# Kernel optimization log

Hardware: AMD Instinct MI355X
Metric: run time of the kernel (lower is better)

## Reference

```python
import jax, jax.numpy as jnp
import numpy as np

G, N, E = 4, 50000, 800000
F_IN, HID, OUT = 64, 128, 64


def setup_inputs() -> dict:
    key = jax.random.key(0)
    ks = jax.random.split(key, 4)
    x = jax.random.normal(ks[0], (G, N, F_IN), dtype=jnp.float32)
    edge_index = jax.random.randint(ks[1], (G, 2, E), 0, N)
    W1 = jax.random.normal(ks[2], (G, F_IN, HID), dtype=jnp.float32) / np.sqrt(F_IN).astype(np.float32)
    b1 = jnp.zeros((G, HID), dtype=jnp.float32)
    W2 = jax.random.normal(ks[3], (G, HID, OUT), dtype=jnp.float32) / np.sqrt(HID).astype(np.float32)
    b2 = jnp.zeros((G, OUT), dtype=jnp.float32)
    return {"x": x, "edge_index": edge_index, "W1": W1, "b1": b1, "W2": W2, "b2": b2}


def gcn_conv(x, src, dst, W, b):
    # PyG GCNConv: add self loops, symmetric norm D^-1/2 (A+I) D^-1/2, then XW + b
    n = x.shape[0]
    loop = jnp.arange(n)
    s = jnp.concatenate([src, loop])  # [E+N]
    d = jnp.concatenate([dst, loop])
    deg = jax.ops.segment_sum(jnp.ones_like(s, dtype=x.dtype), d, num_segments=n)
    dinv = jax.lax.rsqrt(deg)  # deg >= 1 because of self loops
    norm = dinv[s] * dinv[d]  # [E+N]
    h = x @ W  # [N, F_out]
    msg = h[s] * norm[:, None]  # edge-wise gather (memory-bound)
    out = jax.ops.segment_sum(msg, d, num_segments=n)  # scatter-add
    return out + b


def reference(x, edge_index, W1, b1, W2, b2):
    def per_graph(xg, eg, w1, b1g, w2, b2g):
        src, dst = eg[0], eg[1]
        h = jax.nn.elu(gcn_conv(xg, src, dst, w1, b1g))
        h = jax.nn.elu(gcn_conv(h, src, dst, w2, b2g))
        return h  # [N, OUT]

    out = jax.vmap(per_graph)(x, edge_index, W1, b1, W2, b2)  # [G, N, OUT]
    return out.reshape(G * N, OUT)  # torch.cat over graphs along dim 0
```

## Files before the change

### kernel.cpp

```cpp
#include <hip/hip_runtime.h>
#include <cstdint>

constexpr int G = 4, N = 50000, E = 800000;
constexpr int FIN = 64, HID = 128, FOUT = 64;
constexpr int NB = (N + 1023) / 1024;

constexpr int PB = 64;
constexpr int CP = E / PB;
constexpr int NBK = (N + 255) / 256;

typedef unsigned short ushort;
typedef _Float16 f16;

__device__ __forceinline__ ushort f2h(float f) {
  f16 h = (f16)f;
  return __builtin_bit_cast(ushort, h);
}
__device__ __forceinline__ float h2f(ushort u) {
  f16 h = __builtin_bit_cast(f16, u);
  return (float)h;
}

__device__ __forceinline__ void xcd_map(int b, int& g, int& chunk) {
  int xcd = b & 7;
  int sub = b >> 3;
  g = xcd >> 1;
  chunk = (xcd & 1) * 6250 + sub;
}

__global__ void k_x2h(const float4* __restrict__ X, const float* __restrict__ dinv,
                      ushort4* __restrict__ Xh, int n4) {
  int i = blockIdx.x * blockDim.x + threadIdx.x;
  if (i >= n4) return;
  float sc = dinv[i >> 4];
  float4 v = X[i];
  ushort4 o = {f2h(sc * v.x), f2h(sc * v.y), f2h(sc * v.z), f2h(sc * v.w)};
  Xh[i] = o;
}


__global__ __launch_bounds__(256) void k_phist(const int* __restrict__ ei,
                                               int* __restrict__ PH) {
  __shared__ int h[NBK];
  int pb = blockIdx.x, g = blockIdx.y;
  for (int i = threadIdx.x; i < NBK; i += 256) h[i] = 0;
  __syncthreads();
  const int4* dst4 = (const int4*)(ei + (size_t)g * 2 * E + E + (size_t)pb * CP);
  for (int i = threadIdx.x; i < CP / 4; i += 256) {
    int4 d = dst4[i];
    atomicAdd(&h[d.x >> 8], 1);
    atomicAdd(&h[d.y >> 8], 1);
    atomicAdd(&h[d.z >> 8], 1);
    atomicAdd(&h[d.w >> 8], 1);
  }
  __syncthreads();
  for (int i = threadIdx.x; i < NBK; i += 256)
    PH[((size_t)g * NBK + i) * PB + pb] = h[i];
}

__global__ void k_pscan(const int* __restrict__ PH, int* __restrict__ POFF,
                        int* __restrict__ BB) {
  int g = blockIdx.x, k = threadIdx.x;
  int tot = 0;
  if (k < NBK) {
#pragma unroll 8
    for (int pb = 0; pb < PB; ++pb) tot += PH[((size_t)g * NBK + k) * PB + pb];
  }
  __shared__ int sm[256];
  sm[k] = tot;
  __syncthreads();
  for (int off = 1; off < 256; off <<= 1) {
    int v = (k >= off) ? sm[k - off] : 0;
    __syncthreads();
    sm[k] += v;
    __syncthreads();
  }
  int excl = sm[k] - tot;
  if (k < NBK) {
    BB[g * (NBK + 1) + k] = excl;
    if (k == NBK - 1) BB[g * (NBK + 1) + NBK] = excl + tot;
    int run = excl;
#pragma unroll 8
    for (int pb = 0; pb < PB; ++pb) {
      POFF[((size_t)g * NBK + k) * PB + pb] = run;
      run += PH[((size_t)g * NBK + k) * PB + pb];
    }
  }
}

__global__ __launch_bounds__(256) void k_part(const int* __restrict__ ei,
                                              const int* __restrict__ POFF,
                                              unsigned* __restrict__ pairs) {
  __shared__ int off[NBK];
  __shared__ int rk[NBK];
  int pb = blockIdx.x, g = blockIdx.y;
  for (int i = threadIdx.x; i < NBK; i += 256) {
    off[i] = POFF[((size_t)g * NBK + i) * PB + pb];
    rk[i] = 0;
  }
  __syncthreads();
  const int* base = ei + (size_t)g * 2 * E + (size_t)pb * CP;
  const int4* s4 = (const int4*)base;
  const int4* d4 = (const int4*)(base + E);
  unsigned* pg = pairs + (size_t)g * E;
  for (int i = threadIdx.x; i < CP / 4; i += 256) {
    int4 s = s4[i], d = d4[i];
    int sv[4] = {s.x, s.y, s.z, s.w};
    int dv[4] = {d.x, d.y, d.z, d.w};
#pragma unroll
    for (int k = 0; k < 4; ++k) {
      int b = dv[k] >> 8;
      int r = atomicAdd(&rk[b], 1);
      pg[off[b] + r] = (unsigned)sv[k] | ((unsigned)(dv[k] & 255) << 16);
    }
  }
}

__global__ __launch_bounds__(256) void k_bcnt(const unsigned* __restrict__ pairs,
                                              const int* __restrict__ BB,
                                              int* __restrict__ cnt) {
  __shared__ int h[256];
  int k = blockIdx.x, g = blockIdx.y;
  h[threadIdx.x] = 0;
  __syncthreads();
  int lo = BB[g * (NBK + 1) + k], hi = BB[g * (NBK + 1) + k + 1];
  const unsigned* pg = pairs + (size_t)g * E;
  for (int i = lo + (int)threadIdx.x; i < hi; i += 256)
    atomicAdd(&h[(pg[i] >> 16) & 255], 1);
  __syncthreads();
  int n0 = k << 8;
  int nn = min(256, N - n0);
  if ((int)threadIdx.x < nn) cnt[g * N + n0 + threadIdx.x] = h[threadIdx.x];
}

__global__ __launch_bounds__(256) void k_place(const unsigned* __restrict__ pairs,
                                               const int* __restrict__ BB,
                                               const int* __restrict__ rowptr,
                                               int* __restrict__ col) {
  __shared__ int rp[256];
  __shared__ int rk[256];
  int k = blockIdx.x, g = blockIdx.y;
  int n0 = k << 8;
  int nn = min(256, N - n0);
  if ((int)threadIdx.x < nn) rp[threadIdx.x] = rowptr[g * (N + 1) + n0 + threadIdx.x];
  rk[threadIdx.x] = 0;
  __syncthreads();
  int lo = BB[g * (NBK + 1) + k], hi = BB[g * (NBK + 1) + k + 1];
  const unsigned* pg = pairs + (size_t)g * E;
  int* cg = col + (size_t)g * E;
  for (int i = lo + (int)threadIdx.x; i < hi; i += 256) {
    unsigned p = pg[i];
    int dl = (p >> 16) & 255;
    int r = atomicAdd(&rk[dl], 1);
    cg[rp[dl] + r] = (int)(p & 0xffffu);
  }
}

__global__ void k_scan_partial(const int* __restrict__ cnt, int* __restrict__ part) {
  int g = blockIdx.y, b = blockIdx.x, tid = threadIdx.x;
  int base = b * 1024 + tid * 4;
  int s = 0;
#pragma unroll
  for (int k = 0; k < 4; ++k) {
    int i = base + k;
    if (i < N) s += cnt[g * N + i];
  }
  __shared__ int sm[256];
  sm[tid] = s;
  __syncthreads();
  for (int off = 128; off > 0; off >>= 1) {
    if (tid < off) sm[tid] += sm[tid + off];
    __syncthreads();
  }
  if (tid == 0) part[g * NB + b] = sm[0];
}

__global__ void k_scan_mid(int* __restrict__ part, int* __restrict__ rowptr) {
  int g = blockIdx.x;
  if (threadIdx.x != 0) return;
  int run = 0;
  for (int b = 0; b < NB; ++b) {
    int t = part[g * NB + b];
    part[g * NB + b] = run;
    run += t;
  }
  rowptr[g * (N + 1) + N] = run;
}

__global__ void k_scan_final(const int* __restrict__ cnt, const int* __restrict__ part,
                             int* __restrict__ rowptr, float* __restrict__ dinv) {
  int g = blockIdx.y, b = blockIdx.x, tid = threadIdx.x;
  int base = b * 1024 + tid * 4;
  int c[4];
  int s = 0;
#pragma unroll
  for (int k = 0; k < 4; ++k) {
    int i = base + k;
    c[k] = (i < N) ? cnt[g * N + i] : 0;
    s += c[k];
  }
  __shared__ int sm[256];
  sm[tid] = s;
  __syncthreads();
  for (int off = 1; off < 256; off <<= 1) {
    int v = (tid >= off) ? sm[tid - off] : 0;
    __syncthreads();
    sm[tid] += v;
    __syncthreads();
  }
  int excl = sm[tid] - s + part[g * NB + b];
#pragma unroll
  for (int k = 0; k < 4; ++k) {
    int i = base + k;
    if (i < N) {
      rowptr[g * (N + 1) + i] = excl;
      dinv[g * N + i] = rsqrtf((float)(c[k] + 1));
    }
    excl += c[k];
  }
}

__global__ __launch_bounds__(256) void k_mlp(const float* __restrict__ X,
                                             const float* __restrict__ W1,
                                             const float* __restrict__ b1,
                                             const float* __restrict__ W2,
                                             const float* __restrict__ dinv,
                                             ushort* __restrict__ H2s) {
  constexpr int K = FIN;
  constexpr int PK = K + 1;
  __shared__ float lds[4 * 32 * 65];
  float* xs = lds;
  int g = blockIdx.y;
  int R0 = blockIdx.x * 64;
  for (int idx = threadIdx.x; idx < 64 * K; idx += 256) {
    int r = idx / K, k = idx - r * K;
    int row = R0 + r;
    xs[r * PK + k] = (row < N) ? X[((size_t)g * N + row) * K + k] : 0.f;
  }
  __syncthreads();
  int wv = threadIdx.x >> 6;
  int lane = threadIdx.x & 63;
  int c0 = __builtin_amdgcn_readfirstlane(wv * 32);
  const float* W1g = W1 + (size_t)g * K * HID;
  const float* xrow = &xs[lane * PK];
  float acc[32];
#pragma unroll
  for (int c = 0; c < 32; ++c) acc[c] = 0.f;
#pragma unroll 4
  for (int k = 0; k < K; ++k) {
    float xv = xrow[k];
#pragma unroll
    for (int c = 0; c < 32; ++c)
      acc[c] = fmaf(xv, W1g[(size_t)k * HID + c0 + c], acc[c]);
  }
#pragma unroll
  for (int c = 0; c < 32; ++c) {
    float v = acc[c] + b1[g * HID + c0 + c];
    acc[c] = v > 0.f ? v : expm1f(v);
  }
  const float* W2g = W2 + (size_t)g * HID * FOUT;
  int rrow = threadIdx.x >> 2;
  int jg = threadIdx.x & 3;
  for (int h = 0; h < 2; ++h) {
    float ph[32];
#pragma unroll
    for (int j = 0; j < 32; ++j) ph[j] = 0.f;
    for (int c = 0; c < 32; ++c) {
      const float* wr = &W2g[(size_t)(c0 + c) * FOUT + h * 32];
      float av = acc[c];
#pragma unroll
      for (int j = 0; j < 32; ++j) ph[j] = fmaf(av, wr[j], ph[j]);
    }
    __syncthreads();
#pragma unroll
    for (int j = 0; j < 32; ++j) lds[wv * 2080 + j * 65 + lane] = ph[j];
    __syncthreads();
    if (R0 + rrow < N) {
      float dd = dinv[g * N + R0 + rrow];
      ushort4 oa, ob;
      {
        int j = jg * 8;
        float s0 = lds[j * 65 + rrow] + lds[2080 + j * 65 + rrow] +
                   lds[4160 + j * 65 + rrow] + lds[6240 + j * 65 + rrow];
        float s1 = lds[(j + 1) * 65 + rrow] + lds[2080 + (j + 1) * 65 + rrow] +
                   lds[4160 + (j + 1) * 65 + rrow] + lds[6240 + (j + 1) * 65 + rrow];
        float s2 = lds[(j + 2) * 65 + rrow] + lds[2080 + (j + 2) * 65 + rrow] +
                   lds[4160 + (j + 2) * 65 + rrow] + lds[6240 + (j + 2) * 65 + rrow];
        float s3 = lds[(j + 3) * 65 + rrow] + lds[2080 + (j + 3) * 65 + rrow] +
                   lds[4160 + (j + 3) * 65 + rrow] + lds[6240 + (j + 3) * 65 + rrow];
        oa = {f2h(s0 * dd), f2h(s1 * dd), f2h(s2 * dd), f2h(s3 * dd)};
        float s4 = lds[(j + 4) * 65 + rrow] + lds[2080 + (j + 4) * 65 + rrow] +
                   lds[4160 + (j + 4) * 65 + rrow] + lds[6240 + (j + 4) * 65 + rrow];
        float s5 = lds[(j + 5) * 65 + rrow] + lds[2080 + (j + 5) * 65 + rrow] +
                   lds[4160 + (j + 5) * 65 + rrow] + lds[6240 + (j + 5) * 65 + rrow];
        float s6 = lds[(j + 6) * 65 + rrow] + lds[2080 + (j + 6) * 65 + rrow] +
                   lds[4160 + (j + 6) * 65 + rrow] + lds[6240 + (j + 6) * 65 + rrow];
        float s7 = lds[(j + 7) * 65 + rrow] + lds[2080 + (j + 7) * 65 + rrow] +
                   lds[4160 + (j + 7) * 65 + rrow] + lds[6240 + (j + 7) * 65 + rrow];
        ob = {f2h(s4 * dd), f2h(s5 * dd), f2h(s6 * dd), f2h(s7 * dd)};
      }
      ushort* dst = H2s + ((size_t)g * N + R0 + rrow) * FOUT + h * 32 + jg * 8;
      *(ushort4*)dst = oa;
      *(ushort4*)(dst + 4) = ob;
    }
  }
}

__device__ __forceinline__ float agg_row(const ushort* __restrict__ hb,
                                         const int* __restrict__ cl, int rs, int re,
                                         int lane, float acc) {
  int j = rs;
  for (; j + 16 <= re; j += 16) {
    int s[16];
#pragma unroll
    for (int k = 0; k < 16; ++k) s[k] = cl[j + k];
    float v[16];
#pragma unroll
    for (int k = 0; k < 16; ++k) v[k] = h2f(hb[(size_t)s[k] * 64 + lane]);
#pragma unroll
    for (int k = 0; k < 16; ++k) acc += v[k];
  }
  for (; j + 8 <= re; j += 8) {
    int s[8];
#pragma unroll
    for (int k = 0; k < 8; ++k) s[k] = cl[j + k];
    float v[8];
#pragma unroll
    for (int k = 0; k < 8; ++k) v[k] = h2f(hb[(size_t)s[k] * 64 + lane]);
#pragma unroll
    for (int k = 0; k < 8; ++k) acc += v[k];
  }
  for (; j < re; ++j) acc += h2f(hb[(size_t)cl[j] * 64 + lane]);
  return acc;
}

template <int F>
__global__ __launch_bounds__(256) void k_agg_in(const ushort* __restrict__ Xh,
                                                const int* __restrict__ rowptr,
                                                const int* __restrict__ col,
                                                const float* __restrict__ dinv,
                                                float* __restrict__ Z) {
  int g, chunk;
  xcd_map(blockIdx.x, g, chunk);
  int d = __builtin_amdgcn_readfirstlane(chunk * 4 + (threadIdx.x >> 6));
  int lane = threadIdx.x & 63;
  const ushort* hb = Xh + (size_t)g * N * F;
  const int* cl = col + (size_t)g * E;
  int rs = rowptr[g * (N + 1) + d];
  int re = rowptr[g * (N + 1) + d + 1];
  float acc = h2f(hb[(size_t)d * F + lane]);
  acc = agg_row(hb, cl, rs, re, lane, acc);
  Z[((size_t)g * N + d) * F + lane] = dinv[g * N + d] * acc;
}

template <int F>
__global__ __launch_bounds__(256) void k_agg_out(const ushort* __restrict__ Hsrc,
                                                 const int* __restrict__ rowptr,
                                                 const int* __restrict__ col,
                                                 const float* __restrict__ dinv,
                                                 const float* __restrict__ bias,
                                                 float* __restrict__ out) {
  int g, chunk;
  xcd_map(blockIdx.x, g, chunk);
  int d = __builtin_amdgcn_readfirstlane(chunk * 4 + (threadIdx.x >> 6));
  int lane = threadIdx.x & 63;
  const ushort* hb = Hsrc + (size_t)g * N * F;
  const int* cl = col + (size_t)g * E;
  int rs = rowptr[g * (N + 1) + d];
  int re = rowptr[g * (N + 1) + d + 1];
  float acc = h2f(hb[(size_t)d * F + lane]);
  acc = agg_row(hb, cl, rs, re, lane, acc);
  float p = acc * dinv[g * N + d] + bias[g * F + lane];
  p = p > 0.f ? p : expm1f(p);
  out[((size_t)g * N + d) * F + lane] = p;
}

extern "C" void kernel_launch(void* const* d_in, const int* in_sizes, int n_in,
                              void* d_out, int out_size, void* d_ws, size_t ws_size,
                              hipStream_t stream) {
  const float* x = (const float*)d_in[0];
  const int* ei = (const int*)d_in[1];
  const float* W1 = (const float*)d_in[2];
  const float* b1 = (const float*)d_in[3];
  const float* W2 = (const float*)d_in[4];
  const float* b2 = (const float*)d_in[5];
  float* out = (float*)d_out;

  char* p = (char*)d_ws;
  auto alloc = [&](size_t bytes) {
    char* r = p;
    p += (bytes + 255) & ~(size_t)255;
    return r;
  };
  int* cnt = (int*)alloc(sizeof(int) * G * N);
  int* rowptr = (int*)alloc(sizeof(int) * G * (N + 1));
  int* part = (int*)alloc(sizeof(int) * G * NB);
  float* dinv = (float*)alloc(sizeof(float) * G * N);
  int* col = (int*)alloc(sizeof(int) * (size_t)G * E);
  float* z = (float*)alloc(sizeof(float) * (size_t)G * N * FIN);
  char* scratch = (char*)alloc((size_t)103 << 20);
  ushort* h2s = (ushort*)z;
  unsigned* pairs = (unsigned*)scratch;
  int* PH = (int*)(scratch + ((size_t)13 << 20));
  int* POFF = (int*)(scratch + ((size_t)14 << 20));
  int* BB = (int*)(scratch + ((size_t)15 << 20));
  ushort* xh = (ushort*)(scratch + ((size_t)32 << 20));

  k_phist<<<dim3(PB, G), 256, 0, stream>>>(ei, PH);
  k_pscan<<<G, 256, 0, stream>>>(PH, POFF, BB);
  k_part<<<dim3(PB, G), 256, 0, stream>>>(ei, POFF, pairs);
  k_bcnt<<<dim3(NBK, G), 256, 0, stream>>>(pairs, BB, cnt);
  dim3 sg(NB, G);
  k_scan_partial<<<sg, 256, 0, stream>>>(cnt, part);
  k_scan_mid<<<G, 64, 0, stream>>>(part, rowptr);
  k_scan_final<<<sg, 256, 0, stream>>>(cnt, part, rowptr, dinv);
  k_place<<<dim3(NBK, G), 256, 0, stream>>>(pairs, BB, rowptr, col);

  k_x2h<<<(G * N * FIN / 4 + 255) / 256, 256, 0, stream>>>(
      (const float4*)x, dinv, (ushort4*)xh, G * N * FIN / 4);

  k_agg_in<FIN><<<(G * N) / 4, 256, 0, stream>>>(xh, rowptr, col, dinv, z);

  dim3 gg((N + 63) / 64, G);
  k_mlp<<<gg, 256, 0, stream>>>(z, W1, b1, W2, dinv, h2s);

  k_agg_out<FOUT><<<(G * N) / 4, 256, 0, stream>>>(h2s, rowptr, col, dinv, b2, out);
}
```

Measured before the change: 483.5 us.

## Stage layer-1 activations in LDS as fp16 and split second GEMM by output columns

In the fused MLP kernel, each wave used to compute a partial product over its 32 hidden channels for all 64 outputs, then reduce the four partials through a large fp32 LDS buffer in two passes. Now each wave writes its ELU-activated hidden values to LDS as packed fp16. Each wave then computes 16 output columns over the full hidden dimension, which removes the cross-wave reduction, one barrier pair and most of the LDS footprint. Launch bounds now ask for 8 blocks per CU to raise occupancy. The hidden activations pass through fp16 before the second matmul, which adds a small precision loss.

```diff
diff --git a/kernel.cpp b/kernel.cpp
--- a/kernel.cpp
+++ b/kernel.cpp
@@ -220,29 +220,29 @@
   }
 }
 
-__global__ __launch_bounds__(256) void k_mlp(const float* __restrict__ X,
-                                             const float* __restrict__ W1,
-                                             const float* __restrict__ b1,
-                                             const float* __restrict__ W2,
-                                             const float* __restrict__ dinv,
-                                             ushort* __restrict__ H2s) {
+__global__ __launch_bounds__(256, 8) void k_mlp(const float* __restrict__ X,
+                                                const float* __restrict__ W1,
+                                                const float* __restrict__ b1,
+                                                const float* __restrict__ W2,
+                                                const float* __restrict__ dinv,
+                                                ushort* __restrict__ H2s) {
   constexpr int K = FIN;
   constexpr int PK = K + 1;
-  __shared__ float lds[4 * 32 * 65];
-  float* xs = lds;
+  __shared__ float lds[64 * PK];
+  ushort* h1s = (ushort*)lds;
   int g = blockIdx.y;
   int R0 = blockIdx.x * 64;
   for (int idx = threadIdx.x; idx < 64 * K; idx += 256) {
-    int r = idx / K, k = idx - r * K;
+    int r = idx >> 6, k = idx & 63;
     int row = R0 + r;
-    xs[r * PK + k] = (row < N) ? X[((size_t)g * N + row) * K + k] : 0.f;
+    lds[r * PK + k] = (row < N) ? X[((size_t)g * N + row) * K + k] : 0.f;
   }
   __syncthreads();
   int wv = threadIdx.x >> 6;
   int lane = threadIdx.x & 63;
   int c0 = __builtin_amdgcn_readfirstlane(wv * 32);
   const float* W1g = W1 + (size_t)g * K * HID;
-  const float* xrow = &xs[lane * PK];
+  const float* xrow = &lds[lane * PK];
   float acc[32];
 #pragma unroll
   for (int c = 0; c < 32; ++c) acc[c] = 0.f;
@@ -258,51 +258,39 @@
     float v = acc[c] + b1[g * HID + c0 + c];
     acc[c] = v > 0.f ? v : expm1f(v);
   }
-  const float* W2g = W2 + (size_t)g * HID * FOUT;
-  int rrow = threadIdx.x >> 2;
-  int jg = threadIdx.x & 3;
-  for (int h = 0; h < 2; ++h) {
-    float ph[32];
-#pragma unroll
-    for (int j = 0; j < 32; ++j) ph[j] = 0.f;
-    for (int c = 0; c < 32; ++c) {
-      const float* wr = &W2g[(size_t)(c0 + c) * FOUT + h * 32];
-      float av = acc[c];
-#pragma unroll
-      for (int j = 0; j < 32; ++j) ph[j] = fmaf(av, wr[j], ph[j]);
-    }
-    __syncthreads();
-#pragma unroll
-    for (int j = 0; j < 32; ++j) lds[wv * 2080 + j * 65 + lane] = ph[j];
-    __syncthreads();
-    if (R0 + rrow < N) {
-      float dd = dinv[g * N + R0 + rrow];
-      ushort4 oa, ob;
-      {
-        int j = jg * 8;
-        float s0 = lds[j * 65 + rrow] + lds[2080 + j * 65 + rrow] +
-                   lds[4160 + j * 65 + rrow] + lds[6240 + j * 65 + rrow];
-        float s1 = lds[(j + 1) * 65 + rrow] + lds[2080 + (j + 1) * 65 + rrow] +
-                   lds[4160 + (j + 1) * 65 + rrow] + lds[6240 + (j + 1) * 65 + rrow];
-        float s2 = lds[(j + 2) * 65 + rrow] + lds[2080 + (j + 2) * 65 + rrow] +
-                   lds[4160 + (j + 2) * 65 + rrow] + lds[6240 + (j + 2) * 65 + rrow];
-        float s3 = lds[(j + 3) * 65 + rrow] + lds[2080 + (j + 3) * 65 + rrow] +
-                   lds[4160 + (j + 3) * 65 + rrow] + lds[6240 + (j + 3) * 65 + rrow];
-        oa = {f2h(s0 * dd), f2h(s1 * dd), f2h(s2 * dd), f2h(s3 * dd)};
-        float s4 = lds[(j + 4) * 65 + rrow] + lds[2080 + (j + 4) * 65 + rrow] +
-                   lds[4160 + (j + 4) * 65 + rrow] + lds[6240 + (j + 4) * 65 + rrow];
-        float s5 = lds[(j + 5) * 65 + rrow] + lds[2080 + (j + 5) * 65 + rrow] +
-                   lds[4160 + (j + 5) * 65 + rrow] + lds[6240 + (j + 5) * 65 + rrow];
-        float s6 = lds[(j + 6) * 65 + rrow] + lds[2080 + (j + 6) * 65 + rrow] +
-                   lds[4160 + (j + 6) * 65 + rrow] + lds[6240 + (j + 6) * 65 + rrow];
-        float s7 = lds[(j + 7) * 65 + rrow] + lds[2080 + (j + 7) * 65 + rrow] +
-                   lds[4160 + (j + 7) * 65 + rrow] + lds[6240 + (j + 7) * 65 + rrow];
-        ob = {f2h(s4 * dd), f2h(s5 * dd), f2h(s6 * dd), f2h(s7 * dd)};
-      }
-      ushort* dst = H2s + ((size_t)g * N + R0 + rrow) * FOUT + h * 32 + jg * 8;
-      *(ushort4*)dst = oa;
-      *(ushort4*)(dst + 4) = ob;
-    }
+  __syncthreads();
+#pragma unroll
+  for (int c2 = 0; c2 < 16; ++c2) {
+    unsigned pk = (unsigned)f2h(acc[2 * c2]) | ((unsigned)f2h(acc[2 * c2 + 1]) << 16);
+    *(unsigned*)&h1s[lane * 130 + c0 + 2 * c2] = pk;
+  }
+  __syncthreads();
+  int j0 = __builtin_amdgcn_readfirstlane(wv * 16);
+  const float* W2g = W2 + (size_t)g * HID * FOUT + j0;
+  float acc2[16];
+#pragma unroll
+  for (int j = 0; j < 16; ++j) acc2[j] = 0.f;
+#pragma unroll 4
+  for (int c = 0; c < HID; c += 2) {
+    unsigned pk = *(const unsigned*)&h1s[lane * 130 + c];
+    float f0 = h2f((ushort)(pk & 0xffffu));
+    float f1 = h2f((ushort)(pk >> 16));
+    const float* w0 = &W2g[(size_t)c * FOUT];
+    const float* w1 = &W2g[(size_t)(c + 1) * FOUT];
+#pragma unroll
+    for (int j = 0; j < 16; ++j) acc2[j] = fmaf(f0, w0[j], acc2[j]);
+#pragma unroll
+    for (int j = 0; j < 16; ++j) acc2[j] = fmaf(f1, w1[j], acc2[j]);
+  }
+  int row = R0 + lane;
+  if (row < N) {
+    float dd = dinv[g * N + row];
+    ushort o[16];
+#pragma unroll
+    for (int j = 0; j < 16; ++j) o[j] = f2h(acc2[j] * dd);
+    ushort* dst = H2s + ((size_t)g * N + row) * FOUT + j0;
+    *(uint4*)dst = *(uint4*)&o[0];
+    *(uint4*)(dst + 8) = *(uint4*)&o[8];
   }
 }
 
```

New measurement: 490.6 us. No clear change (+1.5%).
